# Kernel tuning notes

Measured on AMD Instinct MI355X. Metric: run time of the kernel, lower is better.

## Reference

```python
import jax, jax.numpy as jnp
import numpy as np

B, K, D, N = 256, 1024, 2048, 50000
T = 0.07
MOMENTUM = 0.5
Z = 52580.0  # hardcoded partition-function constant from the source


def setup_inputs() -> dict:
    key = jax.random.key(0)
    k1, k2, k3, k4 = jax.random.split(key, 4)
    x = jax.random.normal(k1, (B, D), dtype=jnp.float32)  # encoder output (pre-normalize)
    y = jax.random.randint(k2, (B,), 0, N)
    idx = jax.random.randint(k3, (B, K), 0, N)
    stdv = 1.0 / np.sqrt(D / 3.0)
    memory = jax.random.uniform(k4, (N, D), dtype=jnp.float32, minval=-stdv, maxval=stdv)
    return {"x": x, "y": y, "idx": idx, "memory": memory}


def reference(x, y, idx, memory):
    # Normalize(2): L2-normalize features per row
    features = x / jnp.linalg.norm(x, axis=1, keepdims=True)  # [B, D]
    # idx.select(1, 0).copy_(y): positive index in column 0
    idx = idx.at[:, 0].set(y)
    # large random-index gather from the memory bank: [B, K, D]
    weight = jnp.take(memory, idx.reshape(-1), axis=0).reshape(B, K, D)
    # batched dot-product (bmm), temperature, exp, normalize by Z
    output = jnp.exp(jnp.einsum("bkd,bd->bk", weight, features) / T) / Z  # [B, K]
    # momentum update of the positive rows (uses pre-update weight[:, 0])
    weight_pos = weight[:, 0, :] * MOMENTUM + features * (1.0 - MOMENTUM)  # [B, D]
    updated = weight_pos / jnp.linalg.norm(weight_pos, axis=1, keepdims=True)
    # index_copy_ scatter back into a clone of the memory bank
    temp = memory.at[y].set(updated)  # [N, D]
    return output, temp
```

## Files before the change

kernel.cpp:

```cpp
#include <hip/hip_runtime.h>
#include <math.h>

#define NB 256
#define NK 1024
#define ND 2048
#define NN 50000
#define BM 64

constexpr float T_INV = 1.0f / 0.07f;
constexpr float Z_INV = 1.0f / 52580.0f;
constexpr float MOM   = 0.5f;

typedef float f32x4 __attribute__((ext_vector_type(4)));
typedef short s16x8 __attribute__((ext_vector_type(8)));
typedef unsigned int u32x4 __attribute__((ext_vector_type(4)));

__device__ __forceinline__ float blk_reduce_sum256(float v, float* sh) {
    #pragma unroll
    for (int o = 32; o > 0; o >>= 1) v += __shfl_down(v, o, 64);
    int lane = threadIdx.x & 63;
    int wid  = threadIdx.x >> 6;
    if (lane == 0) sh[wid] = v;
    __syncthreads();
    float s = sh[0] + sh[1] + sh[2] + sh[3];
    __syncthreads();
    return s;
}

__device__ __forceinline__ unsigned f2bf_rne(float f) {
    unsigned u = __float_as_uint(f);
    return (u + 0x7fffu + ((u >> 16) & 1u)) >> 16;
}

__global__ void k_feat(const float* __restrict__ x, float* __restrict__ feat,
                       unsigned int* __restrict__ featb) {
    __shared__ float sh[4];
    int b = blockIdx.x;
    int t = threadIdx.x;
    const float4* xr = (const float4*)(x + (size_t)b * ND);
    float4 v0 = xr[t];
    float4 v1 = xr[t + 256];
    float ss = v0.x*v0.x + v0.y*v0.y + v0.z*v0.z + v0.w*v0.w
             + v1.x*v1.x + v1.y*v1.y + v1.z*v1.z + v1.w*v1.w;
    float s = blk_reduce_sum256(ss, sh);
    float r = rsqrtf(s);
    v0.x*=r; v0.y*=r; v0.z*=r; v0.w*=r;
    v1.x*=r; v1.y*=r; v1.z*=r; v1.w*=r;
    float4* fr = (float4*)(feat + (size_t)b * ND);
    fr[t]       = v0;
    fr[t + 256] = v1;
    unsigned int* fb = featb + (size_t)b * (ND / 2);
    fb[2*t]           = f2bf_rne(v0.x) | (f2bf_rne(v0.y) << 16);
    fb[2*t + 1]       = f2bf_rne(v0.z) | (f2bf_rne(v0.w) << 16);
    fb[2*(t+256)]     = f2bf_rne(v1.x) | (f2bf_rne(v1.y) << 16);
    fb[2*(t+256) + 1] = f2bf_rne(v1.z) | (f2bf_rne(v1.w) << 16);
}

template<bool COPY>
__launch_bounds__(256)
__global__ void k_gemm(const float* __restrict__ mem, const short* __restrict__ featb,
                       float* __restrict__ S, float* __restrict__ temp) {
    const int wave = threadIdx.x >> 6;
    const int lane = threadIdx.x & 63;
    const int rlo  = lane & 15;
    const int khi  = lane >> 4;
    const int n0   = blockIdx.x * BM;

    const float* aptr[4];
    #pragma unroll
    for (int m = 0; m < 4; ++m) {
        int r = n0 + m * 16 + rlo;
        if (r >= NN) r = NN - 1;
        aptr[m] = mem + (size_t)r * ND + khi * 8;
    }
    const short* bptr[4];
    #pragma unroll
    for (int j = 0; j < 4; ++j) {
        int c = wave * 64 + j * 16 + rlo;
        bptr[j] = featb + (size_t)c * ND + khi * 8;
    }
    const int crow = n0 + (threadIdx.x >> 2);
    const int ccol = (threadIdx.x & 3) * 8;
    const bool cok = COPY && (crow < NN);
    const float4* csrc = (const float4*)(mem  + (size_t)crow * ND + ccol);
    float4*       cdst = (float4*)(temp + (size_t)crow * ND + ccol);

    f32x4 acc[4][4] = {};

    for (int k0 = 0; k0 < ND; k0 += 32) {
        s16x8 bfr[4];
        #pragma unroll
        for (int j = 0; j < 4; ++j)
            bfr[j] = *(const s16x8*)(bptr[j] + k0);
        s16x8 afr[4];
        #pragma unroll
        for (int m = 0; m < 4; ++m) {
            const float* p = aptr[m] + k0;
            float4 x0 = *(const float4*)p;
            float4 x1 = *(const float4*)(p + 4);
            u32x4 uv = { (__float_as_uint(x0.x) >> 16) | (__float_as_uint(x0.y) & 0xffff0000u),
                         (__float_as_uint(x0.z) >> 16) | (__float_as_uint(x0.w) & 0xffff0000u),
                         (__float_as_uint(x1.x) >> 16) | (__float_as_uint(x1.y) & 0xffff0000u),
                         (__float_as_uint(x1.z) >> 16) | (__float_as_uint(x1.w) & 0xffff0000u) };
            afr[m] = __builtin_bit_cast(s16x8, uv);
        }
        #pragma unroll
        for (int m = 0; m < 4; ++m)
            #pragma unroll
            for (int j = 0; j < 4; ++j)
                acc[m][j] = __builtin_amdgcn_mfma_f32_16x16x32_bf16(afr[m], bfr[j], acc[m][j], 0, 0, 0);
        if (cok) {
            cdst[k0 / 4]     = csrc[k0 / 4];
            cdst[k0 / 4 + 1] = csrc[k0 / 4 + 1];
        }
    }

    const int r_off = (lane >> 4) * 4;
    const int c_off = lane & 15;
    #pragma unroll
    for (int m = 0; m < 4; ++m) {
        int row0 = n0 + m * 16 + r_off;
        #pragma unroll
        for (int j = 0; j < 4; ++j) {
            int col = wave * 64 + j * 16 + c_off;
            #pragma unroll
            for (int r = 0; r < 4; ++r) {
                int row = row0 + r;
                if (row < NN) S[(size_t)row * NB + col] = acc[m][j][r];
            }
        }
    }
}

__global__ void k_out(const float* __restrict__ S, const int* __restrict__ idx,
                      const int* __restrict__ y, float* __restrict__ out) {
    int g = blockIdx.x * 256 + threadIdx.x;
    int b = g >> 10;
    int k = g & (NK - 1);
    int row = (k == 0) ? y[b] : idx[g];
    out[g] = expf(S[(size_t)row * NB + b] * T_INV) * Z_INV;
}

__global__ void k_copy(const float* __restrict__ mem, float* __restrict__ temp) {
    size_t i = (size_t)blockIdx.x * 256 + threadIdx.x;
    ((float4*)temp)[i] = ((const float4*)mem)[i];
}

__global__ void k_scatter(const float* __restrict__ mem, const float* __restrict__ feat,
                          const int* __restrict__ y, float* __restrict__ temp) {
    __shared__ float sh[4];
    int b  = blockIdx.x;
    int yb = y[b];
    for (int b2 = b + 1; b2 < NB; ++b2)
        if (y[b2] == yb) return;
    int t = threadIdx.x;
    const float4* f4 = (const float4*)(feat + (size_t)b * ND);
    const float4* m4 = (const float4*)(mem  + (size_t)yb * ND);
    float4 f0 = f4[t], f1 = f4[t + 256];
    float4 m0 = m4[t], m1 = m4[t + 256];
    float4 w0 = make_float4(m0.x*MOM + f0.x*(1.f-MOM), m0.y*MOM + f0.y*(1.f-MOM),
                            m0.z*MOM + f0.z*(1.f-MOM), m0.w*MOM + f0.w*(1.f-MOM));
    float4 w1 = make_float4(m1.x*MOM + f1.x*(1.f-MOM), m1.y*MOM + f1.y*(1.f-MOM),
                            m1.z*MOM + f1.z*(1.f-MOM), m1.w*MOM + f1.w*(1.f-MOM));
    float ss = w0.x*w0.x + w0.y*w0.y + w0.z*w0.z + w0.w*w0.w
             + w1.x*w1.x + w1.y*w1.y + w1.z*w1.z + w1.w*w1.w;
    float s = blk_reduce_sum256(ss, sh);
    float r = rsqrtf(s);
    float4* d = (float4*)(temp + (size_t)yb * ND);
    d[t]       = make_float4(w0.x*r, w0.y*r, w0.z*r, w0.w*r);
    d[t + 256] = make_float4(w1.x*r, w1.y*r, w1.z*r, w1.w*r);
}

extern "C" void kernel_launch(void* const* d_in, const int* in_sizes, int n_in,
                              void* d_out, int out_size, void* d_ws, size_t ws_size,
                              hipStream_t stream) {
    (void)in_sizes; (void)n_in; (void)out_size;
    const float* x   = (const float*)d_in[0];
    const int*   y   = (const int*)d_in[1];
    const int*   idx = (const int*)d_in[2];
    const float* mem = (const float*)d_in[3];

    float* out  = (float*)d_out;
    float* temp = (float*)d_out + (size_t)NB * NK;

    const size_t szF  = (size_t)NB * ND * sizeof(float);
    const size_t szFB = (size_t)NB * ND * sizeof(short);
    const size_t szS  = (size_t)NN * NB * sizeof(float);
    const int gemm_grid = (NN + BM - 1) / BM;

    if (ws_size >= szF + szFB + szS) {
        float*        feat  = (float*)d_ws;
        unsigned int* featb = (unsigned int*)((char*)d_ws + szF);
        float*        S     = (float*)((char*)d_ws + szF + szFB);
        k_feat<<<NB, 256, 0, stream>>>(x, feat, featb);
        k_gemm<true><<<gemm_grid, 256, 0, stream>>>(mem, (const short*)featb, S, temp);
        k_out<<<(NB * NK) / 256, 256, 0, stream>>>(S, idx, y, out);
        k_scatter<<<NB, 256, 0, stream>>>(mem, feat, y, temp);
    } else {
        float*        feat  = (float*)d_ws;
        unsigned int* featb = (unsigned int*)temp;
        float*        S     = (float*)((char*)temp + szFB);
        k_feat<<<NB, 256, 0, stream>>>(x, feat, featb);
        k_gemm<false><<<gemm_grid, 256, 0, stream>>>(mem, (const short*)featb, S, nullptr);
        k_out<<<(NB * NK) / 256, 256, 0, stream>>>(S, idx, y, out);
        k_copy<<<(NN * ND / 4) / 256, 256, 0, stream>>>(mem, temp);
        k_scatter<<<NB, 256, 0, stream>>>(mem, feat, y, temp);
    }
}
```

Measured before the change: 1.002 ms.

## Stage memory-bank tiles through LDS with async double-buffered global_load_lds

The dense memory-bank GEMM kernel now loads A tiles straight into XOR-swizzled shared memory with global_load_lds, double-buffered across 64-wide K steps, with manual waitcnt and barriers. The bank copy into temp reuses the tile already staged in LDS instead of issuing a second global read. The row tile drops from 64 to 32 to fit the new scheme. This targets the memory-bound streaming of the 400MB bank and its duplicate read for the copy. The trade-off is fragile hand-counted vmcnt values, and B fragments are reused across half as many rows.

New measurement: 812.9 us. 1.23x faster.

```diff
diff --git a/kernel.cpp b/kernel.cpp
--- a/kernel.cpp
+++ b/kernel.cpp
@@ -5,7 +5,8 @@
 #define NK 1024
 #define ND 2048
 #define NN 50000
-#define BM 64
+#define BM 32
+#define NT (ND / 64)
 
 constexpr float T_INV = 1.0f / 0.07f;
 constexpr float Z_INV = 1.0f / 52580.0f;
@@ -14,6 +15,10 @@
 typedef float f32x4 __attribute__((ext_vector_type(4)));
 typedef short s16x8 __attribute__((ext_vector_type(8)));
 typedef unsigned int u32x4 __attribute__((ext_vector_type(4)));
+
+#define AS1 __attribute__((address_space(1)))
+#define AS3 __attribute__((address_space(3)))
+#define SB() __builtin_amdgcn_sched_barrier(0)
 
 __device__ __forceinline__ float blk_reduce_sum256(float v, float* sh) {
     #pragma unroll
@@ -30,6 +35,14 @@
 __device__ __forceinline__ unsigned f2bf_rne(float f) {
     unsigned u = __float_as_uint(f);
     return (u + 0x7fffu + ((u >> 16) & 1u)) >> 16;
+}
+
+__device__ __forceinline__ s16x8 pack_bf16(f32x4 a, f32x4 b) {
+    u32x4 uv = { (__float_as_uint(a[0]) >> 16) | (__float_as_uint(a[1]) & 0xffff0000u),
+                 (__float_as_uint(a[2]) >> 16) | (__float_as_uint(a[3]) & 0xffff0000u),
+                 (__float_as_uint(b[0]) >> 16) | (__float_as_uint(b[1]) & 0xffff0000u),
+                 (__float_as_uint(b[2]) >> 16) | (__float_as_uint(b[3]) & 0xffff0000u) };
+    return __builtin_bit_cast(s16x8, uv);
 }
 
 __global__ void k_feat(const float* __restrict__ x, float* __restrict__ feat,
@@ -60,69 +73,121 @@
 __launch_bounds__(256)
 __global__ void k_gemm(const float* __restrict__ mem, const short* __restrict__ featb,
                        float* __restrict__ S, float* __restrict__ temp) {
-    const int wave = threadIdx.x >> 6;
-    const int lane = threadIdx.x & 63;
+    __shared__ __align__(16) float As[2 * 2048];
+    const int tid  = threadIdx.x;
+    const int wave = tid >> 6;
+    const int lane = tid & 63;
     const int rlo  = lane & 15;
     const int khi  = lane >> 4;
     const int n0   = blockIdx.x * BM;
 
-    const float* aptr[4];
+    const int grow = tid >> 4;
+    const int gcc  = tid & 15;
+    const float* gsrc0;
+    const float* gsrc1;
+    {
+        int r0 = grow,      a0 = n0 + r0; if (a0 >= NN) a0 = NN - 1;
+        int r1 = 16 + grow, a1 = n0 + r1; if (a1 >= NN) a1 = NN - 1;
+        gsrc0 = mem + (size_t)a0 * ND + ((gcc ^ grow) * 4);
+        gsrc1 = mem + (size_t)a1 * ND + ((gcc ^ grow) * 4);
+    }
+
+    const short* bp0 = featb + (size_t)(wave * 64 +  0 + rlo) * ND + khi * 8;
+    const short* bp1 = featb + (size_t)(wave * 64 + 16 + rlo) * ND + khi * 8;
+    const short* bp2 = featb + (size_t)(wave * 64 + 32 + rlo) * ND + khi * 8;
+    const short* bp3 = featb + (size_t)(wave * 64 + 48 + rlo) * ND + khi * 8;
+
+    float* cd0 = nullptr; float* cd1 = nullptr; bool cok0 = false, cok1 = false;
+    if (COPY) {
+        int c0 = n0 + grow;      cok0 = c0 < NN; cd0 = temp + (size_t)c0 * ND + gcc * 4;
+        int c1 = n0 + 16 + grow; cok1 = c1 < NN; cd1 = temp + (size_t)c1 * ND + gcc * 4;
+    }
+
+    const int a0base = rlo * 64;
+    const int a1base = (16 + rlo) * 64;
+    const int cl0 = grow * 64        + ((gcc ^ grow) * 4);
+    const int cl1 = (16 + grow) * 64 + ((gcc ^ grow) * 4);
+
+    f32x4 acc[2][4] = {};
+    s16x8 bfr[8];
+
+    auto GLL = [&](int buf, int kf) {
+        __builtin_amdgcn_global_load_lds((const AS1 void*)(gsrc0 + kf),
+            (AS3 void*)(As + buf * 2048 + tid * 4), 16, 0, 0);
+        __builtin_amdgcn_global_load_lds((const AS1 void*)(gsrc1 + kf),
+            (AS3 void*)(As + buf * 2048 + 1024 + tid * 4), 16, 0, 0);
+    };
+    auto BLOAD = [&](int kf) {
+        #pragma unroll
+        for (int s = 0; s < 2; ++s) {
+            bfr[s*4+0] = *(const s16x8*)(bp0 + kf + s*32);
+            bfr[s*4+1] = *(const s16x8*)(bp1 + kf + s*32);
+            bfr[s*4+2] = *(const s16x8*)(bp2 + kf + s*32);
+            bfr[s*4+3] = *(const s16x8*)(bp3 + kf + s*32);
+        }
+    };
+    auto COMPUTE = [&](int kf, int buf, bool pre) {
+        const float* ab = As + buf * 2048;
+        #pragma unroll
+        for (int s = 0; s < 2; ++s) {
+            const int ch = s * 8 + khi * 2;
+            f32x4 a00 = *(const f32x4*)(ab + a0base + (((ch + 0) ^ rlo) * 4));
+            f32x4 a01 = *(const f32x4*)(ab + a0base + (((ch + 1) ^ rlo) * 4));
+            f32x4 a10 = *(const f32x4*)(ab + a1base + (((ch + 0) ^ rlo) * 4));
+            f32x4 a11 = *(const f32x4*)(ab + a1base + (((ch + 1) ^ rlo) * 4));
+            s16x8 af0 = pack_bf16(a00, a01);
+            s16x8 af1 = pack_bf16(a10, a11);
+            #pragma unroll
+            for (int j = 0; j < 4; ++j) {
+                acc[0][j] = __builtin_amdgcn_mfma_f32_16x16x32_bf16(af0, bfr[s*4+j], acc[0][j], 0, 0, 0);
+                acc[1][j] = __builtin_amdgcn_mfma_f32_16x16x32_bf16(af1, bfr[s*4+j], acc[1][j], 0, 0, 0);
+            }
+        }
+        if (pre) BLOAD(kf + 64);
+        if (COPY) {
+            f32x4 v0 = *(const f32x4*)(ab + cl0);
+            f32x4 v1 = *(const f32x4*)(ab + cl1);
+            if (cok0) *(f32x4*)(cd0 + kf) = v0;
+            if (cok1) *(f32x4*)(cd1 + kf) = v1;
+        }
+    };
+
+    GLL(0, 0);
+    BLOAD(0);
+    asm volatile("s_waitcnt vmcnt(0)" ::: "memory");
+    SB();
+    __builtin_amdgcn_s_barrier();
+    SB();
+    GLL(1, 64);
+    COMPUTE(0, 0, true);
+    for (int t = 1; t < NT - 1; ++t) {
+        const int cur = t & 1;
+        SB();
+        __builtin_amdgcn_s_barrier();
+        SB();
+        GLL(cur ^ 1, (t + 1) * 64);
+        asm volatile("s_waitcnt vmcnt(%0)" :: "n"(COPY ? 12 : 10) : "memory");
+        SB();
+        __builtin_amdgcn_s_barrier();
+        SB();
+        COMPUTE(t * 64, cur, true);
+    }
+    SB();
+    __builtin_amdgcn_s_barrier();
+    SB();
+    asm volatile("s_waitcnt vmcnt(%0)" :: "n"(COPY ? 10 : 8) : "memory");
+    SB();
+    __builtin_amdgcn_s_barrier();
+    SB();
+    COMPUTE((NT - 1) * 64, 1, false);
+
+    const int r_off = khi * 4;
     #pragma unroll
-    for (int m = 0; m < 4; ++m) {
-        int r = n0 + m * 16 + rlo;
-        if (r >= NN) r = NN - 1;
-        aptr[m] = mem + (size_t)r * ND + khi * 8;
-    }
-    const short* bptr[4];
-    #pragma unroll
-    for (int j = 0; j < 4; ++j) {
-        int c = wave * 64 + j * 16 + rlo;
-        bptr[j] = featb + (size_t)c * ND + khi * 8;
-    }
-    const int crow = n0 + (threadIdx.x >> 2);
-    const int ccol = (threadIdx.x & 3) * 8;
-    const bool cok = COPY && (crow < NN);
-    const float4* csrc = (const float4*)(mem  + (size_t)crow * ND + ccol);
-    float4*       cdst = (float4*)(temp + (size_t)crow * ND + ccol);
-
-    f32x4 acc[4][4] = {};
-
-    for (int k0 = 0; k0 < ND; k0 += 32) {
-        s16x8 bfr[4];
-        #pragma unroll
-        for (int j = 0; j < 4; ++j)
-            bfr[j] = *(const s16x8*)(bptr[j] + k0);
-        s16x8 afr[4];
-        #pragma unroll
-        for (int m = 0; m < 4; ++m) {
-            const float* p = aptr[m] + k0;
-            float4 x0 = *(const float4*)p;
-            float4 x1 = *(const float4*)(p + 4);
-            u32x4 uv = { (__float_as_uint(x0.x) >> 16) | (__float_as_uint(x0.y) & 0xffff0000u),
-                         (__float_as_uint(x0.z) >> 16) | (__float_as_uint(x0.w) & 0xffff0000u),
-                         (__float_as_uint(x1.x) >> 16) | (__float_as_uint(x1.y) & 0xffff0000u),
-                         (__float_as_uint(x1.z) >> 16) | (__float_as_uint(x1.w) & 0xffff0000u) };
-            afr[m] = __builtin_bit_cast(s16x8, uv);
-        }
-        #pragma unroll
-        for (int m = 0; m < 4; ++m)
-            #pragma unroll
-            for (int j = 0; j < 4; ++j)
-                acc[m][j] = __builtin_amdgcn_mfma_f32_16x16x32_bf16(afr[m], bfr[j], acc[m][j], 0, 0, 0);
-        if (cok) {
-            cdst[k0 / 4]     = csrc[k0 / 4];
-            cdst[k0 / 4 + 1] = csrc[k0 / 4 + 1];
-        }
-    }
-
-    const int r_off = (lane >> 4) * 4;
-    const int c_off = lane & 15;
-    #pragma unroll
-    for (int m = 0; m < 4; ++m) {
+    for (int m = 0; m < 2; ++m) {
         int row0 = n0 + m * 16 + r_off;
         #pragma unroll
         for (int j = 0; j < 4; ++j) {
-            int col = wave * 64 + j * 16 + c_off;
+            int col = wave * 64 + j * 16 + rlo;
             #pragma unroll
             for (int r = 0; r < 4; ++r) {
                 int row = row0 + r;
@@ -191,18 +256,18 @@
     if (ws_size >= szF + szFB + szS) {
         float*        feat  = (float*)d_ws;
         unsigned int* featb = (unsigned int*)((char*)d_ws + szF);
-        float*        S     = (float*)((char*)d_ws + szF + szFB);
+        float*        Smat  = (float*)((char*)d_ws + szF + szFB);
         k_feat<<<NB, 256, 0, stream>>>(x, feat, featb);
-        k_gemm<true><<<gemm_grid, 256, 0, stream>>>(mem, (const short*)featb, S, temp);
-        k_out<<<(NB * NK) / 256, 256, 0, stream>>>(S, idx, y, out);
+        k_gemm<true><<<gemm_grid, 256, 0, stream>>>(mem, (const short*)featb, Smat, temp);
+        k_out<<<(NB * NK) / 256, 256, 0, stream>>>(Smat, idx, y, out);
         k_scatter<<<NB, 256, 0, stream>>>(mem, feat, y, temp);
     } else {
         float*        feat  = (float*)d_ws;
         unsigned int* featb = (unsigned int*)temp;
-        float*        S     = (float*)((char*)temp + szFB);
+        float*        Smat  = (float*)((char*)temp + szFB);
         k_feat<<<NB, 256, 0, stream>>>(x, feat, featb);
-        k_gemm<false><<<gemm_grid, 256, 0, stream>>>(mem, (const short*)featb, S, nullptr);
-        k_out<<<(NB * NK) / 256, 256, 0, stream>>>(S, idx, y, out);
+        k_gemm<false><<<gemm_grid, 256, 0, stream>>>(mem, (const short*)featb, Smat, nullptr);
+        k_out<<<(NB * NK) / 256, 256, 0, stream>>>(Smat, idx, y, out);
         k_copy<<<(NN * ND / 4) / 256, 256, 0, stream>>>(mem, temp);
         k_scatter<<<NB, 256, 0, stream>>>(mem, feat, y, temp);
     }
```

## Restructure GEMM into single-wave blocks with double-buffered async LDS loads

Applied to the files above, without the earlier changes.

The memory-bank GEMM now runs as one wave per block over 32 rows. Each wave streams fp32 tiles of the bank into a double-buffered, XOR-swizzled LDS area with global_load_lds, using explicit vmcnt waits and sched barriers to overlap the next tile's load with MFMA work. The clone copy into temp is served from the LDS tile instead of a second global read. Each wave now covers all 256 feature columns, so B-fragment loads come straight from global/L2 with more register pressure, and the hand-tuned vmcnt counts are fragile.

Result: no change. 982.5 us (-1.9%).

```diff
diff --git a/kernel.cpp b/kernel.cpp
--- a/kernel.cpp
+++ b/kernel.cpp
@@ -5,7 +5,8 @@
 #define NK 1024
 #define ND 2048
 #define NN 50000
-#define BM 64
+#define BMW 32
+#define NT 32
 
 constexpr float T_INV = 1.0f / 0.07f;
 constexpr float Z_INV = 1.0f / 52580.0f;
@@ -14,6 +15,10 @@
 typedef float f32x4 __attribute__((ext_vector_type(4)));
 typedef short s16x8 __attribute__((ext_vector_type(8)));
 typedef unsigned int u32x4 __attribute__((ext_vector_type(4)));
+
+#define AS1 __attribute__((address_space(1)))
+#define AS3 __attribute__((address_space(3)))
+#define SB() __builtin_amdgcn_sched_barrier(0)
 
 __device__ __forceinline__ float blk_reduce_sum256(float v, float* sh) {
     #pragma unroll
@@ -30,6 +35,14 @@
 __device__ __forceinline__ unsigned f2bf_rne(float f) {
     unsigned u = __float_as_uint(f);
     return (u + 0x7fffu + ((u >> 16) & 1u)) >> 16;
+}
+
+__device__ __forceinline__ s16x8 pack_bf16(f32x4 a, f32x4 b) {
+    u32x4 uv = { (__float_as_uint(a[0]) >> 16) | (__float_as_uint(a[1]) & 0xffff0000u),
+                 (__float_as_uint(a[2]) >> 16) | (__float_as_uint(a[3]) & 0xffff0000u),
+                 (__float_as_uint(b[0]) >> 16) | (__float_as_uint(b[1]) & 0xffff0000u),
+                 (__float_as_uint(b[2]) >> 16) | (__float_as_uint(b[3]) & 0xffff0000u) };
+    return __builtin_bit_cast(s16x8, uv);
 }
 
 __global__ void k_feat(const float* __restrict__ x, float* __restrict__ feat,
@@ -57,76 +70,97 @@
 }
 
 template<bool COPY>
-__launch_bounds__(256)
+__launch_bounds__(64, 2)
 __global__ void k_gemm(const float* __restrict__ mem, const short* __restrict__ featb,
                        float* __restrict__ S, float* __restrict__ temp) {
-    const int wave = threadIdx.x >> 6;
-    const int lane = threadIdx.x & 63;
-    const int rlo  = lane & 15;
-    const int khi  = lane >> 4;
-    const int n0   = blockIdx.x * BM;
-
-    const float* aptr[4];
+    __shared__ __align__(16) float As[2][BMW * 64];
+    const int l   = threadIdx.x;
+    const int rlo = l & 15;
+    const int khi = l >> 4;
+    const int n0  = blockIdx.x * BMW;
+
+    unsigned off[8];
+    bool     cva[8];
     #pragma unroll
-    for (int m = 0; m < 4; ++m) {
-        int r = n0 + m * 16 + rlo;
-        if (r >= NN) r = NN - 1;
-        aptr[m] = mem + (size_t)r * ND + khi * 8;
-    }
-    const short* bptr[4];
+    for (int q = 0; q < 8; ++q) {
+        int rq  = 4 * q + khi;
+        int row = n0 + rq;
+        cva[q]  = row < NN;
+        int rc  = cva[q] ? row : (NN - 1);
+        off[q]  = (unsigned)rc * ND + (unsigned)((rlo ^ (rq & 15)) * 4);
+    }
+
+    const short* bk0 = featb + (size_t)rlo * ND + khi * 8;
+
+    f32x4 acc[2][16] = {};
+
+    auto GLL = [&](int buf, int kf) {
+        #pragma unroll
+        for (int q = 0; q < 8; ++q)
+            __builtin_amdgcn_global_load_lds((const AS1 void*)(mem + (size_t)off[q] + kf),
+                (AS3 void*)(&As[buf][q * 256]), 16, 0, 0);
+    };
+
+    auto BODY = [&](int i, int buf) {
+        const float* ab = As[buf];
+        const int kf = i * 64;
+        if (COPY) {
+            f32x4 cv[8];
+            #pragma unroll
+            for (int q = 0; q < 8; ++q) cv[q] = *(const f32x4*)(ab + q * 256 + l * 4);
+            #pragma unroll
+            for (int q = 0; q < 8; ++q)
+                if (cva[q]) *(f32x4*)(temp + (size_t)off[q] + kf) = cv[q];
+        }
+        const short* bk = bk0 + kf;
+        #pragma unroll
+        for (int s = 0; s < 2; ++s) {
+            const int cb = s * 8 + khi * 2;
+            f32x4 a00 = *(const f32x4*)(ab + rlo * 64        + ((cb + 0) ^ rlo) * 4);
+            f32x4 a01 = *(const f32x4*)(ab + rlo * 64        + ((cb + 1) ^ rlo) * 4);
+            f32x4 a10 = *(const f32x4*)(ab + (16 + rlo) * 64 + ((cb + 0) ^ rlo) * 4);
+            f32x4 a11 = *(const f32x4*)(ab + (16 + rlo) * 64 + ((cb + 1) ^ rlo) * 4);
+            s16x8 af0 = pack_bf16(a00, a01);
+            s16x8 af1 = pack_bf16(a10, a11);
+            #pragma unroll
+            for (int g = 0; g < 16; ++g) {
+                s16x8 bf = *(const s16x8*)(bk + s * 32 + (size_t)g * (16 * ND));
+                acc[0][g] = __builtin_amdgcn_mfma_f32_16x16x32_bf16(af0, bf, acc[0][g], 0, 0, 0);
+                acc[1][g] = __builtin_amdgcn_mfma_f32_16x16x32_bf16(af1, bf, acc[1][g], 0, 0, 0);
+            }
+        }
+    };
+
+    constexpr int W_STEADY = COPY ? 48 : 40;
+    constexpr int W_LAST   = COPY ? 40 : 32;
+
+    GLL(0, 0);
+    SB();
+    GLL(1, 64);
+    asm volatile("s_waitcnt vmcnt(8)" ::: "memory");
+    SB();
+    BODY(0, 0);
+    for (int i = 1; i < NT - 1; ++i) {
+        SB();
+        GLL((i + 1) & 1, (i + 1) * 64);
+        asm volatile("s_waitcnt vmcnt(%0)" :: "n"(W_STEADY) : "memory");
+        SB();
+        BODY(i, i & 1);
+    }
+    SB();
+    asm volatile("s_waitcnt vmcnt(%0)" :: "n"(W_LAST) : "memory");
+    SB();
+    BODY(NT - 1, (NT - 1) & 1);
+
     #pragma unroll
-    for (int j = 0; j < 4; ++j) {
-        int c = wave * 64 + j * 16 + rlo;
-        bptr[j] = featb + (size_t)c * ND + khi * 8;
-    }
-    const int crow = n0 + (threadIdx.x >> 2);
-    const int ccol = (threadIdx.x & 3) * 8;
-    const bool cok = COPY && (crow < NN);
-    const float4* csrc = (const float4*)(mem  + (size_t)crow * ND + ccol);
-    float4*       cdst = (float4*)(temp + (size_t)crow * ND + ccol);
-
-    f32x4 acc[4][4] = {};
-
-    for (int k0 = 0; k0 < ND; k0 += 32) {
-        s16x8 bfr[4];
+    for (int m = 0; m < 2; ++m) {
         #pragma unroll
-        for (int j = 0; j < 4; ++j)
-            bfr[j] = *(const s16x8*)(bptr[j] + k0);
-        s16x8 afr[4];
-        #pragma unroll
-        for (int m = 0; m < 4; ++m) {
-            const float* p = aptr[m] + k0;
-            float4 x0 = *(const float4*)p;
-            float4 x1 = *(const float4*)(p + 4);
-            u32x4 uv = { (__float_as_uint(x0.x) >> 16) | (__float_as_uint(x0.y) & 0xffff0000u),
-                         (__float_as_uint(x0.z) >> 16) | (__float_as_uint(x0.w) & 0xffff0000u),
-                         (__float_as_uint(x1.x) >> 16) | (__float_as_uint(x1.y) & 0xffff0000u),
-                         (__float_as_uint(x1.z) >> 16) | (__float_as_uint(x1.w) & 0xffff0000u) };
-            afr[m] = __builtin_bit_cast(s16x8, uv);
-        }
-        #pragma unroll
-        for (int m = 0; m < 4; ++m)
-            #pragma unroll
-            for (int j = 0; j < 4; ++j)
-                acc[m][j] = __builtin_amdgcn_mfma_f32_16x16x32_bf16(afr[m], bfr[j], acc[m][j], 0, 0, 0);
-        if (cok) {
-            cdst[k0 / 4]     = csrc[k0 / 4];
-            cdst[k0 / 4 + 1] = csrc[k0 / 4 + 1];
-        }
-    }
-
-    const int r_off = (lane >> 4) * 4;
-    const int c_off = lane & 15;
-    #pragma unroll
-    for (int m = 0; m < 4; ++m) {
-        int row0 = n0 + m * 16 + r_off;
-        #pragma unroll
-        for (int j = 0; j < 4; ++j) {
-            int col = wave * 64 + j * 16 + c_off;
-            #pragma unroll
-            for (int r = 0; r < 4; ++r) {
-                int row = row0 + r;
-                if (row < NN) S[(size_t)row * NB + col] = acc[m][j][r];
+        for (int r = 0; r < 4; ++r) {
+            int row = n0 + m * 16 + khi * 4 + r;
+            if (row < NN) {
+                #pragma unroll
+                for (int g = 0; g < 16; ++g)
+                    S[(size_t)row * NB + g * 16 + rlo] = acc[m][g][r];
             }
         }
     }
@@ -186,23 +220,23 @@
     const size_t szF  = (size_t)NB * ND * sizeof(float);
     const size_t szFB = (size_t)NB * ND * sizeof(short);
     const size_t szS  = (size_t)NN * NB * sizeof(float);
-    const int gemm_grid = (NN + BM - 1) / BM;
+    const int gemm_grid = (NN + BMW - 1) / BMW;
 
     if (ws_size >= szF + szFB + szS) {
         float*        feat  = (float*)d_ws;
         unsigned int* featb = (unsigned int*)((char*)d_ws + szF);
-        float*        S     = (float*)((char*)d_ws + szF + szFB);
+        float*        Smat  = (float*)((char*)d_ws + szF + szFB);
         k_feat<<<NB, 256, 0, stream>>>(x, feat, featb);
-        k_gemm<true><<<gemm_grid, 256, 0, stream>>>(mem, (const short*)featb, S, temp);
-        k_out<<<(NB * NK) / 256, 256, 0, stream>>>(S, idx, y, out);
+        k_gemm<true><<<gemm_grid, 64, 0, stream>>>(mem, (const short*)featb, Smat, temp);
+        k_out<<<(NB * NK) / 256, 256, 0, stream>>>(Smat, idx, y, out);
         k_scatter<<<NB, 256, 0, stream>>>(mem, feat, y, temp);
     } else {
         float*        feat  = (float*)d_ws;
         unsigned int* featb = (unsigned int*)temp;
-        float*        S     = (float*)((char*)temp + szFB);
+        float*        Smat  = (float*)((char*)temp + szFB);
         k_feat<<<NB, 256, 0, stream>>>(x, feat, featb);
-        k_gemm<false><<<gemm_grid, 256, 0, stream>>>(mem, (const short*)featb, S, nullptr);
-        k_out<<<(NB * NK) / 256, 256, 0, stream>>>(S, idx, y, out);
+        k_gemm<false><<<gemm_grid, 64, 0, stream>>>(mem, (const short*)featb, Smat, nullptr);
+        k_out<<<(NB * NK) / 256, 256, 0, stream>>>(Smat, idx, y, out);
         k_copy<<<(NN * ND / 4) / 256, 256, 0, stream>>>(mem, temp);
         k_scatter<<<NB, 256, 0, stream>>>(mem, feat, y, temp);
     }
```
